# Performance work log

Hardware: AMD Instinct MI355X
Metric: run time of the kernel (lower is better)

The kernel has to match this reference:

```python
import jax, jax.numpy as jnp
import numpy as np

H, L, N = 128, 8192, 64


def setup_inputs() -> dict:
    key = jax.random.key(0)
    ks = jax.random.split(key, 8)
    u = jax.random.normal(ks[0], (H, L), jnp.float32)
    # lecun_normal-scaled params, per channel
    Ct_ri = jax.random.normal(ks[1], (H, N, 2), jnp.float32) / np.sqrt(N)
    B_raw = jax.random.normal(ks[2], (H, N, 1), jnp.float32) / np.sqrt(N)
    D = jax.random.uniform(ks[3], (H,), jnp.float32)
    lo, hi = np.log(0.001), np.log(0.1)
    log_step = jax.random.uniform(ks[4], (H,), jnp.float32) * (hi - lo) + lo
    n = np.arange(N, dtype=np.float32)
    Lambda_re = jnp.full((N,), -0.5, jnp.float32)
    Lambda_im = jnp.asarray(np.pi * n, jnp.float32)
    p_re = jnp.asarray(np.sqrt(n + 0.5), jnp.float32)
    p_im = jnp.zeros((N,), jnp.float32)
    q_re = jnp.asarray(np.sqrt(n + 0.5), jnp.float32)
    q_im = jnp.zeros((N,), jnp.float32)
    Vc_re = jax.random.normal(ks[5], (N, N), jnp.float32) / np.sqrt(N)
    Vc_im = jax.random.normal(ks[6], (N, N), jnp.float32) / np.sqrt(N)
    return dict(u=u, Ct_ri=Ct_ri, B_raw=B_raw, D=D, log_step=log_step,
                Lambda_re=Lambda_re, Lambda_im=Lambda_im,
                p_re=p_re, p_im=p_im, q_re=q_re, q_im=q_im,
                Vc_re=Vc_re, Vc_im=Vc_im)


def _s4_forward(u, Ct_ri, B_raw, D, log_step,
                Lambda_re, Lambda_im, p_re, p_im, q_re, q_im, Vc_re, Vc_im):
    h, l = u.shape
    Lambda = (Lambda_re + 1j * Lambda_im).astype(jnp.complex64)   # (N,)
    p = (p_re + 1j * p_im).astype(jnp.complex64)                  # (N,)
    q = (q_re + 1j * q_im).astype(jnp.complex64)                  # (N,)
    Vc = (Vc_re + 1j * Vc_im).astype(jnp.complex64)               # (N,N)
    Ct = (Ct_ri[..., 0] + 1j * Ct_ri[..., 1]).astype(jnp.complex64)  # (H,N)
    # B = Vc @ B_raw  per channel -> (H,N)
    B = jnp.einsum('nm,hm->hn', Vc, B_raw[..., 0].astype(jnp.complex64))
    step = jnp.exp(log_step)                                      # (H,)

    # K_gen_DPLR evaluated at the L roots of unity (conv_from_gen)
    omega = jnp.exp(-2j * jnp.pi * (jnp.arange(l) / l)).astype(jnp.complex64)  # (L,)
    g = (2.0 / step)[:, None] * ((1.0 - omega) / (1.0 + omega))[None, :]       # (H,L)
    c = 2.0 / (1.0 + omega)                                                    # (L,)

    # cauchy_dot: sum_n a_n / (g - Lambda_n); reuse one (H,L,N) reciprocal
    recip = 1.0 / (g[:, :, None] - Lambda[None, None, :])          # (H,L,N)
    Ctc = Ct.conj()
    k00 = jnp.einsum('hn,hln->hl', Ctc * B, recip)
    k01 = jnp.einsum('hn,hln->hl', Ctc * p[None, :], recip)
    k10 = jnp.einsum('hn,hln->hl', q.conj()[None, :] * B, recip)
    k11 = jnp.einsum('n,hln->hl', q.conj() * p, recip)
    at_roots = c[None, :] * (k00 - k01 * (1.0 / (1.0 + k11)) * k10)  # (H,L)

    K = jnp.fft.ifft(at_roots, n=l, axis=-1).real                 # (H,L)

    # non_circular_convolution via zero-padded rfft
    ud = jnp.fft.rfft(jnp.pad(u, ((0, 0), (0, l))), axis=-1)
    Kd = jnp.fft.rfft(jnp.pad(K, ((0, 0), (0, l))), axis=-1)
    y = jnp.fft.irfft(ud * Kd, axis=-1)[:, :l]                    # (H,L)
    return y + D[:, None] * u


def reference(u, Ct_ri, B_raw, D, log_step,
              Lambda_re, Lambda_im, p_re, p_im, q_re, q_im, Vc_re, Vc_im):
    return _s4_forward(u, Ct_ri, B_raw, D, log_step,
                       Lambda_re, Lambda_im, p_re, p_im, q_re, q_im,
                       Vc_re, Vc_im)
```

## Files before the change

kernel.cpp:

```cpp
#include <hip/hip_runtime.h>
#include <math.h>

#define H 128
#define L 8192
#define NSTATE 64
#define NTH 1024
#define PI_D 3.14159265358979323846
#define RT2 0.70710678118654752440f

#define W16K_RE 0.99999992646571789f
#define W16K_IM (-3.8349518757139556e-4f)
#define W32K_RE 0.99999998161642898f
#define W32K_IM (-1.9174759731070332e-4f)

typedef float v2f __attribute__((ext_vector_type(2)));

__device__ __forceinline__ v2f pkfma(v2f a, v2f b, v2f c) {
    return __builtin_elementwise_fma(a, b, c);
}
__device__ __forceinline__ v2f pkfma(float a, v2f b, v2f c) {
    v2f av = a; return __builtin_elementwise_fma(av, b, c);
}

__device__ __forceinline__ int SWZ(int e) { return e ^ ((e >> 3) & 7); }
__device__ __forceinline__ int TSW(int j) { return j ^ ((j >> 4) & 15) ^ ((j >> 8) & 15); }
__device__ __forceinline__ int brev13(int x) { return (int)(__brev((unsigned)x) >> 19); }

__device__ __forceinline__ float2 cmul(float2 a, float2 b) {
    return make_float2(a.x * b.x - a.y * b.y, a.x * b.y + a.y * b.x);
}
__device__ __forceinline__ float2 cmulc(float2 w, float2 x) {
    return make_float2(w.x * x.x + w.y * x.y, w.x * x.y - w.y * x.x);
}
__device__ __forceinline__ float2 cadd(float2 a, float2 b) { return make_float2(a.x + b.x, a.y + b.y); }
__device__ __forceinline__ float2 csub(float2 a, float2 b) { return make_float2(a.x - b.x, a.y - b.y); }
__device__ __forceinline__ float2 mnegi(float2 a) { return make_float2(a.y, -a.x); }
__device__ __forceinline__ float2 mposi(float2 a) { return make_float2(-a.y, a.x); }

template<int SIGMA>
__device__ __forceinline__ void dif_pass1(float2* __restrict__ A,
                                          const float2* __restrict__ tw, int tid) {
    const int m1 = 2048 / SIGMA;
    #pragma unroll
    for (int rep = 0; rep < 2; ++rep) {
        int q = tid + rep * NTH;
        int r = q & (SIGMA - 1);
        int b = ((q & ~(SIGMA - 1)) << 2) | r;
        float2 w1 = tw[TSW(r * m1)];
        float2 w2 = cmul(w1, w1);
        float2 w1b = mnegi(w1);
        int i0 = SWZ(b), i1 = SWZ(b + SIGMA), i2 = SWZ(b + 2 * SIGMA), i3 = SWZ(b + 3 * SIGMA);
        float2 x0 = A[i0], x1 = A[i1], x2 = A[i2], x3 = A[i3];
        float2 y0 = cadd(x0, x2), y2 = cmul(csub(x0, x2), w1);
        float2 y1 = cadd(x1, x3), y3 = cmul(csub(x1, x3), w1b);
        A[i0] = cadd(y0, y1); A[i1] = cmul(csub(y0, y1), w2);
        A[i2] = cadd(y2, y3); A[i3] = cmul(csub(y2, y3), w2);
    }
}

template<int SIGMA>
__device__ __forceinline__ void dit_pass1(float2* __restrict__ A,
                                          const float2* __restrict__ tw, int tid) {
    const int m1 = 2048 / SIGMA;
    #pragma unroll
    for (int rep = 0; rep < 2; ++rep) {
        int q = tid + rep * NTH;
        int r = q & (SIGMA - 1);
        int b = ((q & ~(SIGMA - 1)) << 2) | r;
        float2 v1 = tw[TSW(r * m1)];
        float2 v2 = cmul(v1, v1);
        int i0 = SWZ(b), i1 = SWZ(b + SIGMA), i2 = SWZ(b + 2 * SIGMA), i3 = SWZ(b + 3 * SIGMA);
        float2 x0 = A[i0], x1 = A[i1], x2 = A[i2], x3 = A[i3];
        float2 t1 = cmulc(v2, x1);
        float2 y0 = cadd(x0, t1), y1 = csub(x0, t1);
        float2 t3 = cmulc(v2, x3);
        float2 y2 = cadd(x2, t3), y3 = csub(x2, t3);
        float2 u2 = cmulc(v1, y2);
        A[i0] = cadd(y0, u2); A[i2] = csub(y0, u2);
        float2 u3 = mposi(cmulc(v1, y3));
        A[i1] = cadd(y1, u3); A[i3] = csub(y1, u3);
    }
}

__device__ __forceinline__ void dif_first_load(float2* __restrict__ A,
                                               const float2* __restrict__ tw,
                                               int tid, const float* __restrict__ ur,
                                               int type) {
    #pragma unroll
    for (int rep = 0; rep < 2; ++rep) {
        int q = tid + rep * NTH;
        float u0 = ur[q], u1 = ur[q + 2048], u2v = ur[q + 4096], u3v = ur[q + 6144];
        float2 x0, x1, x2, x3;
        if (type == 0) {
            x0 = make_float2(u0, 0.f); x1 = make_float2(u1, 0.f);
            x2 = make_float2(u2v, 0.f); x3 = make_float2(u3v, 0.f);
        } else {
            int hq = q >> 1;
            float2 wa = tw[TSW(hq)];
            float2 wb = tw[TSW(hq + 1024)];
            float2 adj = (q & 1) ? make_float2(W16K_RE, W16K_IM) : make_float2(1.f, 0.f);
            wa = cmul(wa, adj); wb = cmul(wb, adj);
            float2 wc = mnegi(wa), wd = mnegi(wb);
            x0 = make_float2(u0 * wa.x, u0 * wa.y);
            x1 = make_float2(u1 * wb.x, u1 * wb.y);
            x2 = make_float2(u2v * wc.x, u2v * wc.y);
            x3 = make_float2(u3v * wd.x, u3v * wd.y);
        }
        float2 w1 = tw[TSW(q)];
        float2 w2 = cmul(w1, w1);
        float2 w1b = mnegi(w1);
        float2 y0 = cadd(x0, x2), y2 = cmul(csub(x0, x2), w1);
        float2 y1 = cadd(x1, x3), y3 = cmul(csub(x1, x3), w1b);
        A[SWZ(q)]        = cadd(y0, y1);
        A[SWZ(q + 2048)] = cmul(csub(y0, y1), w2);
        A[SWZ(q + 4096)] = cadd(y2, y3);
        A[SWZ(q + 6144)] = cmul(csub(y2, y3), w2);
    }
}

template<bool SP>
__device__ __forceinline__ void dit_last_store(const float2* __restrict__ A,
                                               const float2* __restrict__ tw,
                                               int tid, int type,
                                               const float* __restrict__ ur, float Dh,
                                               float* __restrict__ orow,
                                               float* __restrict__ yrow) {
    const float sc = 0.5f / (float)L;
    #pragma unroll
    for (int rep = 0; rep < 2; ++rep) {
        int q = tid + rep * NTH;
        float2 v1 = tw[TSW(q)];
        float2 v2 = cmul(v1, v1);
        float2 x0 = A[SWZ(q)], x1 = A[SWZ(q + 2048)];
        float2 x2 = A[SWZ(q + 4096)], x3 = A[SWZ(q + 6144)];
        float2 t1 = cmulc(v2, x1);
        float2 y0 = cadd(x0, t1), y1 = csub(x0, t1);
        float2 t3 = cmulc(v2, x3);
        float2 y2 = cadd(x2, t3), y3 = csub(x2, t3);
        float2 u2c = cmulc(v1, y2);
        float2 z0 = cadd(y0, u2c), z2 = csub(y0, u2c);
        float2 u3c = mposi(cmulc(v1, y3));
        float2 z1 = cadd(y1, u3c), z3 = csub(y1, u3c);
        float v0, vv1, vv2, vv3;
        if (type == 0) {
            v0  = z0.x * sc + Dh * ur[q];
            vv1 = z1.x * sc + Dh * ur[q + 2048];
            vv2 = z2.x * sc + Dh * ur[q + 4096];
            vv3 = z3.x * sc + Dh * ur[q + 6144];
        } else {
            int hq = q >> 1;
            float2 wa = tw[TSW(hq)];
            float2 wb = tw[TSW(hq + 1024)];
            float2 adj = (q & 1) ? make_float2(W16K_RE, W16K_IM) : make_float2(1.f, 0.f);
            wa = cmul(wa, adj); wb = cmul(wb, adj);
            float2 wc = mnegi(wa), wd = mnegi(wb);
            v0  = (wa.x * z0.x + wa.y * z0.y) * sc;
            vv1 = (wb.x * z1.x + wb.y * z1.y) * sc;
            vv2 = (wc.x * z2.x + wc.y * z2.y) * sc;
            vv3 = (wd.x * z3.x + wd.y * z3.y) * sc;
        }
        float* dst = (type == 0) ? orow : (SP ? yrow : orow);
        if constexpr (SP) {
            dst[q] = v0; dst[q + 2048] = vv1; dst[q + 4096] = vv2; dst[q + 6144] = vv3;
        } else {
            atomicAdd(&dst[q], v0); atomicAdd(&dst[q + 2048], vv1);
            atomicAdd(&dst[q + 4096], vv2); atomicAdd(&dst[q + 6144], vv3);
        }
    }
}

template<int P>
__device__ __forceinline__ void cauchy_chunk(
    const int type, const int tid, const float two_over_step,
    const float2* __restrict__ tw,
    const float4* __restrict__ wq, const float2* __restrict__ wr,
    const float4* __restrict__ wp,
    float* __restrict__ specRe, float* __restrict__ specIm)
{
    const float2 W16K = make_float2(W16K_RE, W16K_IM);
    const float2 W32K = make_float2(W32K_RE, W32K_IM);
    float tk0, tk1;
    v2f gv;
    #pragma unroll
    for (int e = 0; e < 2; ++e) {
        int k = brev13(8 * tid + 2 * P + e);
        float2 w;
        if (e == 0) {
            w = tw[TSW(k >> 1)];
        } else {
            float2 t0 = tw[TSW((k >> 1) - 2048)];
            w = make_float2(t0.y, -t0.x);
        }
        if (k & 1) w = cmul(w, W16K);
        if (type)  w = cmul(w, W32K);
        float t = -w.y * __builtin_amdgcn_rcpf(w.x);
        t = fminf(fmaxf(t, -3.0e7f), 3.0e7f);
        if (e == 0) { tk0 = t; gv.x = two_over_step * t; }
        else        { tk1 = t; gv.y = two_over_step * t; }
    }
    v2f A00x = 0.f, A00y = 0.f, A01x = 0.f, A01y = 0.f;
    v2f A10x = 0.f, A10y = 0.f, A11x = 0.f, A11y = 0.f;
    #pragma unroll 2
    for (int n = 0; n < NSTATE; ++n) {
        float4 qv = wq[n];
        float2 rv = wr[n];
        float4 pv = wp[n];
        v2f dim = gv - pv.z;
        v2f dre2 = pv.y;
        v2f den = pkfma(dim, dim, dre2);
        float rp = __builtin_amdgcn_rcpf(den.x * den.y);
        v2f inv; inv.x = den.y * rp; inv.y = den.x * rp;
        v2f rre = pv.x * inv;
        v2f rip = dim * inv;
        A00x = pkfma(qv.x, rre, pkfma( qv.y, rip, A00x));
        A00y = pkfma(qv.y, rre, pkfma(-qv.x, rip, A00y));
        A01x = pkfma(qv.z, rre, pkfma( qv.w, rip, A01x));
        A01y = pkfma(qv.w, rre, pkfma(-qv.z, rip, A01y));
        A10x = pkfma(rv.x, rre, pkfma( rv.y, rip, A10x));
        A10y = pkfma(rv.y, rre, pkfma(-rv.x, rip, A10y));
        A11x = pkfma( pv.w, rre, A11x);
        A11y = pkfma(-pv.w, rip, A11y);
    }
    #pragma unroll
    for (int e = 0; e < 2; ++e) {
        float2 a00 = make_float2(e ? A00x.y : A00x.x, e ? A00y.y : A00y.x);
        float2 a01 = make_float2(e ? A01x.y : A01x.x, e ? A01y.y : A01y.x);
        float2 a10 = make_float2(e ? A10x.y : A10x.x, e ? A10y.y : A10y.x);
        float2 a11 = make_float2(e ? A11x.y : A11x.x, e ? A11y.y : A11y.x);
        float tt = e ? tk1 : tk0;
        float2 den1 = make_float2(1.0f + a11.x, a11.y);
        float invd = 1.0f / (den1.x * den1.x + den1.y * den1.y);
        float2 qn = cmul(a01, a10);
        float2 dv = make_float2((qn.x * den1.x + qn.y * den1.y) * invd,
                                (qn.y * den1.x - qn.x * den1.y) * invd);
        float2 tmp = make_float2(a00.x - dv.x, a00.y - dv.y);
        float2 s = cmul(make_float2(1.0f, tt), tmp);
        int j = 2 * P + e;
        specRe[j * NTH + tid] = s.x;
        specIm[j * NTH + tid] = s.y;
    }
}

__global__ __launch_bounds__(NSTATE)
void s4_prep(const float* __restrict__ Ct_ri, const float* __restrict__ B_raw,
             const float* __restrict__ Lre_g, const float* __restrict__ Lim_g,
             const float* __restrict__ p_re, const float* __restrict__ p_im,
             const float* __restrict__ q_re, const float* __restrict__ q_im,
             const float* __restrict__ Vc_re, const float* __restrict__ Vc_im,
             char* __restrict__ ws)
{
    const int h = blockIdx.x, n = threadIdx.x;
    float2 Bc = make_float2(0.f, 0.f);
    for (int m = 0; m < NSTATE; ++m) {
        float br = B_raw[h * NSTATE + m];
        Bc.x += Vc_re[n * NSTATE + m] * br;
        Bc.y += Vc_im[n * NSTATE + m] * br;
    }
    float2 Ctc = make_float2(Ct_ri[(h * NSTATE + n) * 2 + 0],
                             -Ct_ri[(h * NSTATE + n) * 2 + 1]);
    float2 pc = make_float2(p_re[n], p_im[n]);
    float2 qc = make_float2(q_re[n], -q_im[n]);
    float2 w00 = cmul(Ctc, Bc);
    float2 w01 = cmul(Ctc, pc);
    float2 w10 = cmul(qc, Bc);
    float2 w11 = cmul(qc, pc);
    float dre = -Lre_g[n];
    float4* wq = (float4*)ws;
    float2* wr = (float2*)(ws + (size_t)H * NSTATE * 16);
    float4* wp = (float4*)(ws + (size_t)H * NSTATE * 24);
    wq[h * NSTATE + n] = make_float4(w00.x, w00.y, w01.x, w01.y);
    wr[h * NSTATE + n] = make_float2(w10.x, w10.y);
    wp[h * NSTATE + n] = make_float4(dre, dre * dre, Lim_g[n], w11.x);
}

__global__ __launch_bounds__(256)
void s4_combine(float4* __restrict__ out, const float4* __restrict__ yneg) {
    int i = blockIdx.x * 256 + threadIdx.x;
    float4 a = out[i], b = yneg[i];
    out[i] = make_float4(a.x + b.x, a.y + b.y, a.z + b.z, a.w + b.w);
}

extern __shared__ char smem_raw[];

template<bool WG, bool SP>
__global__ __launch_bounds__(NTH)
void s4_split_kernel(const float* __restrict__ u,
                     const float* __restrict__ Ct_ri,
                     const float* __restrict__ B_raw,
                     const float* __restrict__ Dp,
                     const float* __restrict__ log_step,
                     const float* __restrict__ Lre_g,
                     const float* __restrict__ Lim_g,
                     const float* __restrict__ p_re,
                     const float* __restrict__ p_im,
                     const float* __restrict__ q_re,
                     const float* __restrict__ q_im,
                     const float* __restrict__ Vc_re,
                     const float* __restrict__ Vc_im,
                     const char* __restrict__ wsw,
                     float* __restrict__ yneg,
                     float* __restrict__ out)
{
    float2* bufA   = (float2*)smem_raw;
    float2* tw     = bufA + L;
    float*  specRe = (float*)(tw + 2048);
    float*  specIm = specRe + L;
    float4* wq4    = (float4*)(specIm + L);
    float2* wr2    = (float2*)(wq4 + NSTATE);
    float4* wp4    = (float4*)(wr2 + NSTATE);

    const int bid  = blockIdx.x;
    const int type = bid >> 7;
    const int h    = bid & (H - 1);
    const int tid  = threadIdx.x;

    for (int j = tid; j < 2048; j += NTH) {
        double a = -2.0 * PI_D * (double)j / (double)L;
        tw[TSW(j)] = make_float2((float)cos(a), (float)sin(a));
    }
    const float4* wqp; const float2* wrp; const float4* wpp;
    if constexpr (WG) {
        wqp = (const float4*)wsw + (size_t)h * NSTATE;
        wrp = (const float2*)(wsw + (size_t)H * NSTATE * 16) + (size_t)h * NSTATE;
        wpp = (const float4*)(wsw + (size_t)H * NSTATE * 24) + (size_t)h * NSTATE;
    } else {
        if (tid < NSTATE) {
            int n = tid;
            float2 Bc = make_float2(0.f, 0.f);
            for (int m = 0; m < NSTATE; ++m) {
                float br = B_raw[h * NSTATE + m];
                Bc.x += Vc_re[n * NSTATE + m] * br;
                Bc.y += Vc_im[n * NSTATE + m] * br;
            }
            float2 Ctc = make_float2(Ct_ri[(h * NSTATE + n) * 2 + 0],
                                     -Ct_ri[(h * NSTATE + n) * 2 + 1]);
            float2 pc = make_float2(p_re[n], p_im[n]);
            float2 qc = make_float2(q_re[n], -q_im[n]);
            float2 w00 = cmul(Ctc, Bc);
            float2 w01 = cmul(Ctc, pc);
            float2 w10 = cmul(qc, Bc);
            float2 w11 = cmul(qc, pc);
            float dre = -Lre_g[n];
            wq4[n] = make_float4(w00.x, w00.y, w01.x, w01.y);
            wr2[n] = make_float2(w10.x, w10.y);
            wp4[n] = make_float4(dre, dre * dre, Lim_g[n], w11.x);
        }
        wqp = wq4; wrp = wr2; wpp = wp4;
    }
    __syncthreads();

    const float step = expf(log_step[h]);
    const float two_over_step = 2.0f / step;
    const float Dh = Dp[h];
    const float* ur = u + (size_t)h * L;

    dif_first_load(bufA, tw, tid, ur, type);
    cauchy_chunk<0>(type, tid, two_over_step, tw, wqp, wrp, wpp, specRe, specIm);
    __syncthreads();
    dif_pass1<512>(bufA, tw, tid);
    cauchy_chunk<1>(type, tid, two_over_step, tw, wqp, wrp, wpp, specRe, specIm);
    __syncthreads();
    dif_pass1<128>(bufA, tw, tid);
    cauchy_chunk<2>(type, tid, two_over_step, tw, wqp, wrp, wpp, specRe, specIm);
    __syncthreads();
    dif_pass1<32>(bufA, tw, tid);
    cauchy_chunk<3>(type, tid, two_over_step, tw, wqp, wrp, wpp, specRe, specIm);
    __syncthreads();
    dif_pass1<8>(bufA, tw, tid);    __syncthreads();

    {
        const int base = tid * 8;
        float2 x0 = bufA[SWZ(base + 0)], x1 = bufA[SWZ(base + 1)];
        float2 x2 = bufA[SWZ(base + 2)], x3 = bufA[SWZ(base + 3)];
        float2 x4 = bufA[SWZ(base + 4)], x5 = bufA[SWZ(base + 5)];
        float2 x6 = bufA[SWZ(base + 6)], x7 = bufA[SWZ(base + 7)];
        float2 a0 = cadd(x0, x4), a1 = cadd(x1, x5), a2 = cadd(x2, x6), a3 = cadd(x3, x7);
        float2 s0 = csub(x0, x4), s1 = csub(x1, x5), s2 = csub(x2, x6), s3 = csub(x3, x7);
        float2 b0 = s0;
        float2 b1 = cmul(s1, make_float2(RT2, -RT2));
        float2 b2 = mnegi(s2);
        float2 b3 = cmul(s3, make_float2(-RT2, -RT2));
        float2 c0 = cadd(a0, a2), c2 = csub(a0, a2);
        float2 c1 = cadd(a1, a3), c3 = mnegi(csub(a1, a3));
        float2 d0 = cadd(b0, b2), d2 = csub(b0, b2);
        float2 d1 = cadd(b1, b3), d3 = mnegi(csub(b1, b3));
        float2 y0 = cadd(c0, c1), y1 = csub(c0, c1);
        float2 y2 = cadd(c2, c3), y3 = csub(c2, c3);
        float2 y4 = cadd(d0, d1), y5 = csub(d0, d1);
        float2 y6 = cadd(d2, d3), y7 = csub(d2, d3);
        y0 = cmul(y0, make_float2(specRe[0 * NTH + tid], specIm[0 * NTH + tid]));
        y1 = cmul(y1, make_float2(specRe[1 * NTH + tid], specIm[1 * NTH + tid]));
        y2 = cmul(y2, make_float2(specRe[2 * NTH + tid], specIm[2 * NTH + tid]));
        y3 = cmul(y3, make_float2(specRe[3 * NTH + tid], specIm[3 * NTH + tid]));
        y4 = cmul(y4, make_float2(specRe[4 * NTH + tid], specIm[4 * NTH + tid]));
        y5 = cmul(y5, make_float2(specRe[5 * NTH + tid], specIm[5 * NTH + tid]));
        y6 = cmul(y6, make_float2(specRe[6 * NTH + tid], specIm[6 * NTH + tid]));
        y7 = cmul(y7, make_float2(specRe[7 * NTH + tid], specIm[7 * NTH + tid]));
        float2 e0 = cadd(y0, y1), e1 = csub(y0, y1), e2 = cadd(y2, y3), e3 = csub(y2, y3);
        float2 e4 = cadd(y4, y5), e5 = csub(y4, y5), e6 = cadd(y6, y7), e7 = csub(y6, y7);
        float2 f0 = cadd(e0, e2), f2 = csub(e0, e2);
        float2 ti = mposi(e3); float2 f1 = cadd(e1, ti), f3 = csub(e1, ti);
        float2 f4 = cadd(e4, e6), f6 = csub(e4, e6);
        float2 tj = mposi(e7); float2 f5 = cadd(e5, tj), f7 = csub(e5, tj);
        float2 g4 = f4;
        float2 g5 = cmul(make_float2(RT2, RT2), f5);
        float2 g6 = mposi(f6);
        float2 g7 = cmul(make_float2(-RT2, RT2), f7);
        bufA[SWZ(base + 0)] = cadd(f0, g4); bufA[SWZ(base + 4)] = csub(f0, g4);
        bufA[SWZ(base + 1)] = cadd(f1, g5); bufA[SWZ(base + 5)] = csub(f1, g5);
        bufA[SWZ(base + 2)] = cadd(f2, g6); bufA[SWZ(base + 6)] = csub(f2, g6);
        bufA[SWZ(base + 3)] = cadd(f3, g7); bufA[SWZ(base + 7)] = csub(f3, g7);
    }
    __syncthreads();

    dit_pass1<8>(bufA, tw, tid);    __syncthreads();
    dit_pass1<32>(bufA, tw, tid);   __syncthreads();
    dit_pass1<128>(bufA, tw, tid);  __syncthreads();
    dit_pass1<512>(bufA, tw, tid);  __syncthreads();
    dit_last_store<SP>(bufA, tw, tid, type, ur, Dh,
                       out + (size_t)h * L,
                       SP ? (yneg + (size_t)h * L) : nullptr);
}

extern "C" void kernel_launch(void* const* d_in, const int* in_sizes, int n_in,
                              void* d_out, int out_size, void* d_ws, size_t ws_size,
                              hipStream_t stream) {
    (void)in_sizes; (void)n_in; (void)out_size;
    const float* u        = (const float*)d_in[0];
    const float* Ct_ri    = (const float*)d_in[1];
    const float* B_raw    = (const float*)d_in[2];
    const float* Dp       = (const float*)d_in[3];
    const float* log_step = (const float*)d_in[4];
    const float* Lre      = (const float*)d_in[5];
    const float* Lim      = (const float*)d_in[6];
    const float* p_re     = (const float*)d_in[7];
    const float* p_im     = (const float*)d_in[8];
    const float* q_re     = (const float*)d_in[9];
    const float* q_im     = (const float*)d_in[10];
    const float* Vc_re    = (const float*)d_in[11];
    const float* Vc_im    = (const float*)d_in[12];
    float* out = (float*)d_out;

    const size_t needW = (size_t)H * NSTATE * (16 + 8 + 16);
    const size_t needY = needW + (size_t)H * L * sizeof(float);
    const bool wg = ws_size >= needW;
    const bool sp = ws_size >= needY;

    char*  wsw  = (char*)d_ws;
    float* yneg = (float*)((char*)d_ws + needW);

    const size_t smemW = (size_t)(L + 2048) * sizeof(float2)
                       + (size_t)2 * L * sizeof(float);
    const size_t smemL = smemW + NSTATE * (16 + 8 + 16);

    if (wg) {
        s4_prep<<<dim3(H), dim3(NSTATE), 0, stream>>>(
            Ct_ri, B_raw, Lre, Lim, p_re, p_im, q_re, q_im, Vc_re, Vc_im, wsw);
        if (sp) {
            hipFuncSetAttribute((const void*)s4_split_kernel<true, true>,
                                hipFuncAttributeMaxDynamicSharedMemorySize, (int)smemW);
            s4_split_kernel<true, true><<<dim3(2 * H), dim3(NTH), smemW, stream>>>(
                u, Ct_ri, B_raw, Dp, log_step, Lre, Lim,
                p_re, p_im, q_re, q_im, Vc_re, Vc_im, wsw, yneg, out);
            s4_combine<<<dim3((H * L) / (256 * 4)), dim3(256), 0, stream>>>(
                (float4*)out, (const float4*)yneg);
        } else {
            hipMemsetAsync(out, 0, (size_t)H * L * sizeof(float), stream);
            hipFuncSetAttribute((const void*)s4_split_kernel<true, false>,
                                hipFuncAttributeMaxDynamicSharedMemorySize, (int)smemW);
            s4_split_kernel<true, false><<<dim3(2 * H), dim3(NTH), smemW, stream>>>(
                u, Ct_ri, B_raw, Dp, log_step, Lre, Lim,
                p_re, p_im, q_re, q_im, Vc_re, Vc_im, wsw, nullptr, out);
        }
    } else {
        hipMemsetAsync(out, 0, (size_t)H * L * sizeof(float), stream);
        hipFuncSetAttribute((const void*)s4_split_kernel<false, false>,
                            hipFuncAttributeMaxDynamicSharedMemorySize, (int)smemL);
        s4_split_kernel<false, false><<<dim3(2 * H), dim3(NTH), smemL, stream>>>(
            u, Ct_ri, B_raw, Dp, log_step, Lre, Lim,
            p_re, p_im, q_re, q_im, Vc_re, Vc_im, nullptr, nullptr, out);
    }
}
```

Before: 79.58 us.

## Replace radix-4 FFT passes with radix-8 passes to cut LDS round trips

The middle stages of the forward and inverse FFT move from radix-4 passes (two butterflies per thread) to radix-8 passes (one 8-point butterfly per thread). The central spectral-multiply block shrinks from a radix-8 to a radix-4 pair to keep the stage factorization consistent. This removes one shared-memory pass and one barrier on each side of the transform, cutting LDS traffic and synchronization. In exchange each thread holds more registers and does more twiddle multiplies per butterfly, which could lower occupancy.

```diff
diff --git a/kernel.cpp b/kernel.cpp
--- a/kernel.cpp
+++ b/kernel.cpp
@@ -38,48 +38,67 @@
 __device__ __forceinline__ float2 mposi(float2 a) { return make_float2(-a.y, a.x); }
 
 template<int SIGMA>
-__device__ __forceinline__ void dif_pass1(float2* __restrict__ A,
-                                          const float2* __restrict__ tw, int tid) {
-    const int m1 = 2048 / SIGMA;
-    #pragma unroll
-    for (int rep = 0; rep < 2; ++rep) {
-        int q = tid + rep * NTH;
-        int r = q & (SIGMA - 1);
-        int b = ((q & ~(SIGMA - 1)) << 2) | r;
-        float2 w1 = tw[TSW(r * m1)];
-        float2 w2 = cmul(w1, w1);
-        float2 w1b = mnegi(w1);
-        int i0 = SWZ(b), i1 = SWZ(b + SIGMA), i2 = SWZ(b + 2 * SIGMA), i3 = SWZ(b + 3 * SIGMA);
-        float2 x0 = A[i0], x1 = A[i1], x2 = A[i2], x3 = A[i3];
-        float2 y0 = cadd(x0, x2), y2 = cmul(csub(x0, x2), w1);
-        float2 y1 = cadd(x1, x3), y3 = cmul(csub(x1, x3), w1b);
-        A[i0] = cadd(y0, y1); A[i1] = cmul(csub(y0, y1), w2);
-        A[i2] = cadd(y2, y3); A[i3] = cmul(csub(y2, y3), w2);
-    }
+__device__ __forceinline__ void dif_r8(float2* __restrict__ A,
+                                       const float2* __restrict__ tw, int tid) {
+    const int M1 = 1024 / SIGMA;
+    int r = tid & (SIGMA - 1);
+    int b = ((tid & ~(SIGMA - 1)) << 3) | r;
+    float2 w1 = tw[TSW(r * M1)];
+    float2 w2 = cmul(w1, w1);
+    float2 w4 = cmul(w2, w2);
+    float2 wj1 = cmul(w1, make_float2(RT2, -RT2));
+    float2 wj2 = mnegi(w1);
+    float2 wj3 = cmul(w1, make_float2(-RT2, -RT2));
+    int i0 = SWZ(b), i1 = SWZ(b + SIGMA), i2 = SWZ(b + 2 * SIGMA), i3 = SWZ(b + 3 * SIGMA);
+    int i4 = SWZ(b + 4 * SIGMA), i5 = SWZ(b + 5 * SIGMA), i6 = SWZ(b + 6 * SIGMA), i7 = SWZ(b + 7 * SIGMA);
+    float2 x0 = A[i0], x1 = A[i1], x2 = A[i2], x3 = A[i3];
+    float2 x4 = A[i4], x5 = A[i5], x6 = A[i6], x7 = A[i7];
+    float2 a0 = cadd(x0, x4), a1 = cadd(x1, x5), a2 = cadd(x2, x6), a3 = cadd(x3, x7);
+    float2 s0 = cmul(csub(x0, x4), w1);
+    float2 s1 = cmul(csub(x1, x5), wj1);
+    float2 s2 = cmul(csub(x2, x6), wj2);
+    float2 s3 = cmul(csub(x3, x7), wj3);
+    float2 c0 = cadd(a0, a2), c1 = cadd(a1, a3);
+    float2 c2 = cmul(csub(a0, a2), w2);
+    float2 c3 = cmul(mnegi(csub(a1, a3)), w2);
+    float2 d0 = cadd(s0, s2), d1 = cadd(s1, s3);
+    float2 d2 = cmul(csub(s0, s2), w2);
+    float2 d3 = cmul(mnegi(csub(s1, s3)), w2);
+    A[i0] = cadd(c0, c1); A[i1] = cmul(csub(c0, c1), w4);
+    A[i2] = cadd(c2, c3); A[i3] = cmul(csub(c2, c3), w4);
+    A[i4] = cadd(d0, d1); A[i5] = cmul(csub(d0, d1), w4);
+    A[i6] = cadd(d2, d3); A[i7] = cmul(csub(d2, d3), w4);
 }
 
 template<int SIGMA>
-__device__ __forceinline__ void dit_pass1(float2* __restrict__ A,
-                                          const float2* __restrict__ tw, int tid) {
-    const int m1 = 2048 / SIGMA;
-    #pragma unroll
-    for (int rep = 0; rep < 2; ++rep) {
-        int q = tid + rep * NTH;
-        int r = q & (SIGMA - 1);
-        int b = ((q & ~(SIGMA - 1)) << 2) | r;
-        float2 v1 = tw[TSW(r * m1)];
-        float2 v2 = cmul(v1, v1);
-        int i0 = SWZ(b), i1 = SWZ(b + SIGMA), i2 = SWZ(b + 2 * SIGMA), i3 = SWZ(b + 3 * SIGMA);
-        float2 x0 = A[i0], x1 = A[i1], x2 = A[i2], x3 = A[i3];
-        float2 t1 = cmulc(v2, x1);
-        float2 y0 = cadd(x0, t1), y1 = csub(x0, t1);
-        float2 t3 = cmulc(v2, x3);
-        float2 y2 = cadd(x2, t3), y3 = csub(x2, t3);
-        float2 u2 = cmulc(v1, y2);
-        A[i0] = cadd(y0, u2); A[i2] = csub(y0, u2);
-        float2 u3 = mposi(cmulc(v1, y3));
-        A[i1] = cadd(y1, u3); A[i3] = csub(y1, u3);
-    }
+__device__ __forceinline__ void dit_r8(float2* __restrict__ A,
+                                       const float2* __restrict__ tw, int tid) {
+    const int M1 = 1024 / SIGMA;
+    int r = tid & (SIGMA - 1);
+    int b = ((tid & ~(SIGMA - 1)) << 3) | r;
+    float2 w1 = tw[TSW(r * M1)];
+    float2 w2 = cmul(w1, w1);
+    float2 w4 = cmul(w2, w2);
+    float2 wj1 = cmul(w1, make_float2(RT2, -RT2));
+    float2 wj2 = mnegi(w1);
+    float2 wj3 = cmul(w1, make_float2(-RT2, -RT2));
+    int i0 = SWZ(b), i1 = SWZ(b + SIGMA), i2 = SWZ(b + 2 * SIGMA), i3 = SWZ(b + 3 * SIGMA);
+    int i4 = SWZ(b + 4 * SIGMA), i5 = SWZ(b + 5 * SIGMA), i6 = SWZ(b + 6 * SIGMA), i7 = SWZ(b + 7 * SIGMA);
+    float2 x0 = A[i0], x1 = A[i1], x2 = A[i2], x3 = A[i3];
+    float2 x4 = A[i4], x5 = A[i5], x6 = A[i6], x7 = A[i7];
+    float2 t;
+    t = cmulc(w4, x1); float2 e0 = cadd(x0, t), e1 = csub(x0, t);
+    t = cmulc(w4, x3); float2 e2 = cadd(x2, t), e3 = csub(x2, t);
+    t = cmulc(w4, x5); float2 e4 = cadd(x4, t), e5 = csub(x4, t);
+    t = cmulc(w4, x7); float2 e6 = cadd(x6, t), e7 = csub(x6, t);
+    t = cmulc(w2, e2);        float2 f0 = cadd(e0, t), f2 = csub(e0, t);
+    t = mposi(cmulc(w2, e3)); float2 f1 = cadd(e1, t), f3 = csub(e1, t);
+    t = cmulc(w2, e6);        float2 f4 = cadd(e4, t), f6 = csub(e4, t);
+    t = mposi(cmulc(w2, e7)); float2 f5 = cadd(e5, t), f7 = csub(e5, t);
+    t = cmulc(w1, f4);  A[i0] = cadd(f0, t); A[i4] = csub(f0, t);
+    t = cmulc(wj1, f5); A[i1] = cadd(f1, t); A[i5] = csub(f1, t);
+    t = cmulc(wj2, f6); A[i2] = cadd(f2, t); A[i6] = csub(f2, t);
+    t = cmulc(wj3, f7); A[i3] = cadd(f3, t); A[i7] = csub(f3, t);
 }
 
 __device__ __forceinline__ void dif_first_load(float2* __restrict__ A,
@@ -357,66 +376,44 @@
     dif_first_load(bufA, tw, tid, ur, type);
     cauchy_chunk<0>(type, tid, two_over_step, tw, wqp, wrp, wpp, specRe, specIm);
     __syncthreads();
-    dif_pass1<512>(bufA, tw, tid);
+    dif_r8<256>(bufA, tw, tid);
     cauchy_chunk<1>(type, tid, two_over_step, tw, wqp, wrp, wpp, specRe, specIm);
     __syncthreads();
-    dif_pass1<128>(bufA, tw, tid);
+    dif_r8<32>(bufA, tw, tid);
     cauchy_chunk<2>(type, tid, two_over_step, tw, wqp, wrp, wpp, specRe, specIm);
     __syncthreads();
-    dif_pass1<32>(bufA, tw, tid);
+    dif_r8<4>(bufA, tw, tid);
     cauchy_chunk<3>(type, tid, two_over_step, tw, wqp, wrp, wpp, specRe, specIm);
     __syncthreads();
-    dif_pass1<8>(bufA, tw, tid);    __syncthreads();
 
     {
         const int base = tid * 8;
-        float2 x0 = bufA[SWZ(base + 0)], x1 = bufA[SWZ(base + 1)];
-        float2 x2 = bufA[SWZ(base + 2)], x3 = bufA[SWZ(base + 3)];
-        float2 x4 = bufA[SWZ(base + 4)], x5 = bufA[SWZ(base + 5)];
-        float2 x6 = bufA[SWZ(base + 6)], x7 = bufA[SWZ(base + 7)];
-        float2 a0 = cadd(x0, x4), a1 = cadd(x1, x5), a2 = cadd(x2, x6), a3 = cadd(x3, x7);
-        float2 s0 = csub(x0, x4), s1 = csub(x1, x5), s2 = csub(x2, x6), s3 = csub(x3, x7);
-        float2 b0 = s0;
-        float2 b1 = cmul(s1, make_float2(RT2, -RT2));
-        float2 b2 = mnegi(s2);
-        float2 b3 = cmul(s3, make_float2(-RT2, -RT2));
-        float2 c0 = cadd(a0, a2), c2 = csub(a0, a2);
-        float2 c1 = cadd(a1, a3), c3 = mnegi(csub(a1, a3));
-        float2 d0 = cadd(b0, b2), d2 = csub(b0, b2);
-        float2 d1 = cadd(b1, b3), d3 = mnegi(csub(b1, b3));
-        float2 y0 = cadd(c0, c1), y1 = csub(c0, c1);
-        float2 y2 = cadd(c2, c3), y3 = csub(c2, c3);
-        float2 y4 = cadd(d0, d1), y5 = csub(d0, d1);
-        float2 y6 = cadd(d2, d3), y7 = csub(d2, d3);
-        y0 = cmul(y0, make_float2(specRe[0 * NTH + tid], specIm[0 * NTH + tid]));
-        y1 = cmul(y1, make_float2(specRe[1 * NTH + tid], specIm[1 * NTH + tid]));
-        y2 = cmul(y2, make_float2(specRe[2 * NTH + tid], specIm[2 * NTH + tid]));
-        y3 = cmul(y3, make_float2(specRe[3 * NTH + tid], specIm[3 * NTH + tid]));
-        y4 = cmul(y4, make_float2(specRe[4 * NTH + tid], specIm[4 * NTH + tid]));
-        y5 = cmul(y5, make_float2(specRe[5 * NTH + tid], specIm[5 * NTH + tid]));
-        y6 = cmul(y6, make_float2(specRe[6 * NTH + tid], specIm[6 * NTH + tid]));
-        y7 = cmul(y7, make_float2(specRe[7 * NTH + tid], specIm[7 * NTH + tid]));
-        float2 e0 = cadd(y0, y1), e1 = csub(y0, y1), e2 = cadd(y2, y3), e3 = csub(y2, y3);
-        float2 e4 = cadd(y4, y5), e5 = csub(y4, y5), e6 = cadd(y6, y7), e7 = csub(y6, y7);
-        float2 f0 = cadd(e0, e2), f2 = csub(e0, e2);
-        float2 ti = mposi(e3); float2 f1 = cadd(e1, ti), f3 = csub(e1, ti);
-        float2 f4 = cadd(e4, e6), f6 = csub(e4, e6);
-        float2 tj = mposi(e7); float2 f5 = cadd(e5, tj), f7 = csub(e5, tj);
-        float2 g4 = f4;
-        float2 g5 = cmul(make_float2(RT2, RT2), f5);
-        float2 g6 = mposi(f6);
-        float2 g7 = cmul(make_float2(-RT2, RT2), f7);
-        bufA[SWZ(base + 0)] = cadd(f0, g4); bufA[SWZ(base + 4)] = csub(f0, g4);
-        bufA[SWZ(base + 1)] = cadd(f1, g5); bufA[SWZ(base + 5)] = csub(f1, g5);
-        bufA[SWZ(base + 2)] = cadd(f2, g6); bufA[SWZ(base + 6)] = csub(f2, g6);
-        bufA[SWZ(base + 3)] = cadd(f3, g7); bufA[SWZ(base + 7)] = csub(f3, g7);
-    }
-    __syncthreads();
-
-    dit_pass1<8>(bufA, tw, tid);    __syncthreads();
-    dit_pass1<32>(bufA, tw, tid);   __syncthreads();
-    dit_pass1<128>(bufA, tw, tid);  __syncthreads();
-    dit_pass1<512>(bufA, tw, tid);  __syncthreads();
+        #pragma unroll
+        for (int un = 0; un < 2; ++un) {
+            int p0 = base + un * 4;
+            int j0 = SWZ(p0), j1 = SWZ(p0 + 1), j2 = SWZ(p0 + 2), j3 = SWZ(p0 + 3);
+            float2 x0 = bufA[j0], x1 = bufA[j1], x2 = bufA[j2], x3 = bufA[j3];
+            float2 a0 = cadd(x0, x2), a1 = cadd(x1, x3);
+            float2 s0 = csub(x0, x2), s1 = mnegi(csub(x1, x3));
+            float2 y0 = cadd(a0, a1), y1 = csub(a0, a1);
+            float2 y2 = cadd(s0, s1), y3 = csub(s0, s1);
+            int sj = un * 4;
+            y0 = cmul(y0, make_float2(specRe[(sj + 0) * NTH + tid], specIm[(sj + 0) * NTH + tid]));
+            y1 = cmul(y1, make_float2(specRe[(sj + 1) * NTH + tid], specIm[(sj + 1) * NTH + tid]));
+            y2 = cmul(y2, make_float2(specRe[(sj + 2) * NTH + tid], specIm[(sj + 2) * NTH + tid]));
+            y3 = cmul(y3, make_float2(specRe[(sj + 3) * NTH + tid], specIm[(sj + 3) * NTH + tid]));
+            float2 e0 = cadd(y0, y1), e1 = csub(y0, y1);
+            float2 e2 = cadd(y2, y3), e3 = csub(y2, y3);
+            float2 ti = mposi(e3);
+            bufA[j0] = cadd(e0, e2); bufA[j2] = csub(e0, e2);
+            bufA[j1] = cadd(e1, ti); bufA[j3] = csub(e1, ti);
+        }
+    }
+    __syncthreads();
+
+    dit_r8<4>(bufA, tw, tid);   __syncthreads();
+    dit_r8<32>(bufA, tw, tid);  __syncthreads();
+    dit_r8<256>(bufA, tw, tid); __syncthreads();
     dit_last_store<SP>(bufA, tw, tid, type, ur, Dh,
                        out + (size_t)h * L,
                        SP ? (yneg + (size_t)h * L) : nullptr);
```

Result: faster. 77.86 us (-2.2%).
